# Performance work log

Hardware: AMD Instinct MI355X
Metric: run time of the kernel (lower is better)

## Reference

```python
import jax, jax.numpy as jnp
import numpy as np

N, E, DIN, DOUT, NNZ = 8192, 4096, 256, 128, 65536
TEMP = float(DOUT) ** 0.5
NEG = -1e9


def setup_inputs() -> dict:
    key = jax.random.key(0)
    ks = jax.random.split(key, 8)
    stdv = 1.0 / np.sqrt(DOUT)
    u = lambda k, shp: jax.random.uniform(k, shp, jnp.float32, -stdv, stdv)
    x = jax.random.normal(ks[0], (N, DIN), jnp.float32)
    nodes = jax.random.randint(ks[1], (NNZ,), 0, N, jnp.int32)
    edges = jax.random.randint(ks[2], (NNZ,), 0, E, jnp.int32)
    hyperedge_index = jnp.stack([nodes, edges])  # [2, nnz]
    return {
        "x": x,
        "weight": u(ks[3], (DIN, DOUT)),   # transfer weight
        "weight2": u(ks[4], (DIN, DOUT)),
        "weight3": u(ks[5], (DOUT, DOUT)),
        "bias": u(ks[6], (DOUT,)),
        "q_ctx": u(ks[7], (DOUT,)),        # word_context.weight[0]
        "hyperedge_index": hyperedge_index,
        "num_nodes": N,
        "num_edges": E,
    }


def reference(x, weight, weight2, weight3, bias, q_ctx, hyperedge_index, num_nodes, num_edges):
    # dense incidence H[node, edge] = 1  (hyperedge_preprocess)
    H = jnp.zeros((num_nodes, num_edges), x.dtype).at[
        hyperedge_index[0], hyperedge_index[1]].set(1.0)
    adj = H.T                       # [E, N]  (mask / original attention for attn1)

    x4 = x @ weight2                # [N, D]  x_4att
    xt = x @ weight + bias          # [N, D]  transferred features (v of attn1)

    # ---- attention1: query = shared word-context vector, keys = x4 ----
    row = (q_ctx / TEMP) @ x4.T                    # [N] (q1 rows are identical)
    scores1 = jnp.where(adj == 0, NEG, row[None, :])  # [E, N]
    att1 = jax.nn.softmax(adj, axis=-1) + jax.nn.softmax(scores1, axis=-1)
    edge = att1 @ xt                               # [E, D]

    att2he = att1.T                                # [N, E]

    # ---- attention2: queries = x4, keys = edge @ W3 ----
    edge4 = edge @ weight3                         # [E, D]
    scores2 = jnp.where(adj.T == 0, NEG, (x4 / TEMP) @ edge4.T)  # [N, E]
    att2hn = jax.nn.softmax(adj.T, axis=-1) + jax.nn.softmax(scores2, axis=-1)

    # ---- fused outer-product attention and output projection ----
    A = att2he @ att2he.T + att2hn @ att2hn.T      # [N, N]
    h_prime_g = jax.nn.elu(A @ x4)                 # [N, D]
    return h_prime_g
```

## Files before the change

kernel.cpp:

```cpp
#include <hip/hip_runtime.h>
#include <math.h>

constexpr int Nn   = 8192;
constexpr int Ee   = 4096;
constexpr int DIN  = 256;
constexpr int DOUT = 128;
constexpr int NNZ  = 65536;
constexpr int EC   = 96;
constexpr int NC   = 48;

#define TEMPR 0.08838834764831845f
#define EM1   1.7182818284590452f

typedef __attribute__((ext_vector_type(8))) short short8;
typedef __attribute__((ext_vector_type(4))) float f32x4;

static __device__ __forceinline__ float wave_sum64(float v) {
#pragma unroll
    for (int m = 32; m; m >>= 1) v += __shfl_xor(v, m, 64);
    return v;
}
static __device__ __forceinline__ float wave_max64(float v) {
#pragma unroll
    for (int m = 32; m; m >>= 1) v = fmaxf(v, __shfl_xor(v, m, 64));
    return v;
}
static __device__ __forceinline__ short f2bf(float f) {
    union { float f; unsigned u; } v; v.f = f;
    const unsigned r = (v.u + 0x7FFFu + ((v.u >> 16) & 1u)) >> 16;
    return (short)r;
}
static __device__ __forceinline__ unsigned packbf2(float a, float b) {
    return ((unsigned)(unsigned short)f2bf(a)) |
           (((unsigned)(unsigned short)f2bf(b)) << 16);
}
static __device__ __forceinline__ float2 unpackbf2(unsigned u) {
    union { unsigned u; float f; } lo, hi;
    lo.u = u << 16; hi.u = u & 0xFFFF0000u;
    return make_float2(lo.f, hi.f);
}

__global__ __launch_bounds__(256) void k_ww3(
    const float* __restrict__ W, const float* __restrict__ W2,
    const float* __restrict__ W3, const float* __restrict__ bias,
    short* __restrict__ W2T, short* __restrict__ WWT, float* __restrict__ bW3,
    uint4* __restrict__ zb, unsigned zTot16)
{
    const int b = blockIdx.x;
    const int t = threadIdx.x;
    if (b < 32) {
        __shared__ float sW[8][128];
        const int r0 = b * 8;
        for (int i = t; i < 1024; i += 256)
            sW[i >> 7][i & 127] = W[(size_t)(r0 + (i >> 7)) * DOUT + (i & 127)];
        __syncthreads();
        const int c  = t & 127;
        const int rh = (t >> 7) * 4;
        float acc[4] = {0.f, 0.f, 0.f, 0.f};
        for (int k = 0; k < 128; ++k) {
            const float w3 = W3[(size_t)k * DOUT + c];
#pragma unroll
            for (int i = 0; i < 4; ++i) acc[i] = fmaf(sW[rh + i][k], w3, acc[i]);
        }
#pragma unroll
        for (int i = 0; i < 4; ++i)
            WWT[(size_t)c * DIN + (r0 + rh + i)] = f2bf(acc[i]);
    } else if (b < 40) {
        const int k0 = (b - 32) * 32;
        for (int i = t; i < 32 * 128; i += 256) {
            const int k = k0 + (i >> 7);
            const int n = i & 127;
            W2T[(size_t)n * DIN + k] = f2bf(W2[(size_t)k * DOUT + n]);
        }
    } else if (b == 40) {
        if (t < 128) {
            float acc = 0.f;
            for (int k = 0; k < 128; ++k)
                acc = fmaf(bias[k], W3[(size_t)k * DOUT + t], acc);
            bW3[t] = acc;
        }
    } else {
        uint4 z; z.x = z.y = z.z = z.w = 0u;
        for (unsigned i = (unsigned)(b - 41) * 256u + t; i < zTot16;
             i += 64u * 256u)
            zb[i] = z;
    }
}

__global__ __launch_bounds__(256) void k_gemm1f(
    const float* __restrict__ x, const short* __restrict__ W2T,
    const short* __restrict__ WWT, const float* __restrict__ bW3,
    const float* __restrict__ q, const int* __restrict__ hidx,
    unsigned* __restrict__ bitmap, int* __restrict__ degE, int* __restrict__ degN,
    int* __restrict__ csrEn, int* __restrict__ csrNe, int* __restrict__ csrNs,
    short* __restrict__ x4b, short* __restrict__ xwb,
    float* __restrict__ rowv)
{
    __shared__ float srow[16];
    const int t    = threadIdx.x;
    const int lane = t & 63;
    const int wv   = t >> 6;
    const int n16  = lane & 15;
    const int quad = lane >> 4;
    const int r0   = blockIdx.x * 16;
    const int n0   = wv * 32;

    const unsigned gid = blockIdx.x * 256 + t;
    if (gid < NNZ) {
        const int n = hidx[gid];
        const int e = hidx[NNZ + gid];
        const unsigned word = (unsigned)n * (unsigned)Ee + (unsigned)e;
        const unsigned bit  = 1u << (word & 31u);
        const unsigned old  = atomicOr(&bitmap[word >> 5], bit);
        if (!(old & bit)) {
            const int pe = atomicAdd(&degE[e], 1);
            if (pe < EC) {
                csrEn[e * EC + pe] = n;
                const int pn = atomicAdd(&degN[n], 1);
                if (pn < NC) {
                    csrNe[n * NC + pn] = e;
                    csrNs[n * NC + pn] = e * EC + pe;
                }
            }
        }
    }

    f32x4 acc4[2], accw[2];
#pragma unroll
    for (int nt = 0; nt < 2; ++nt) {
        acc4[nt] = (f32x4){0.f, 0.f, 0.f, 0.f};
        accw[nt] = (f32x4){0.f, 0.f, 0.f, 0.f};
    }
#pragma unroll
    for (int k0 = 0; k0 < DIN; k0 += 32) {
        const int kb = k0 + quad * 8;
        const float4 xa = *(const float4*)&x[(size_t)(r0 + n16) * DIN + kb];
        const float4 xb = *(const float4*)&x[(size_t)(r0 + n16) * DIN + kb + 4];
        short8 af;
        af[0] = f2bf(xa.x); af[1] = f2bf(xa.y); af[2] = f2bf(xa.z); af[3] = f2bf(xa.w);
        af[4] = f2bf(xb.x); af[5] = f2bf(xb.y); af[6] = f2bf(xb.z); af[7] = f2bf(xb.w);
#pragma unroll
        for (int nt = 0; nt < 2; ++nt) {
            const int col = n0 + nt * 16 + n16;
            const short8 b4 = *(const short8*)&W2T[(size_t)col * DIN + kb];
            const short8 bw = *(const short8*)&WWT[(size_t)col * DIN + kb];
            acc4[nt] = __builtin_amdgcn_mfma_f32_16x16x32_bf16(af, b4, acc4[nt], 0, 0, 0);
            accw[nt] = __builtin_amdgcn_mfma_f32_16x16x32_bf16(af, bw, accw[nt], 0, 0, 0);
        }
    }

    float bwv[2], qv[2];
#pragma unroll
    for (int nt = 0; nt < 2; ++nt) {
        const int col = n0 + nt * 16 + n16;
        bwv[nt] = bW3[col];
        qv[nt]  = q[col];
    }
#pragma unroll
    for (int nt = 0; nt < 2; ++nt) {
        const int col = n0 + nt * 16 + n16;
#pragma unroll
        for (int reg = 0; reg < 4; ++reg) {
            const int row = r0 + quad * 4 + reg;
            x4b[(size_t)row * DOUT + col] = f2bf(acc4[nt][reg]);
            xwb[(size_t)row * DOUT + col] = f2bf(accw[nt][reg] + bwv[nt]);
        }
    }
    float pr[4];
#pragma unroll
    for (int reg = 0; reg < 4; ++reg)
        pr[reg] = qv[0] * acc4[0][reg] + qv[1] * acc4[1][reg];
#pragma unroll
    for (int m = 8; m; m >>= 1) {
#pragma unroll
        for (int reg = 0; reg < 4; ++reg) pr[reg] += __shfl_xor(pr[reg], m, 64);
    }
    if (t < 16) srow[t] = 0.f;
    __syncthreads();
    if (n16 == 0) {
#pragma unroll
        for (int reg = 0; reg < 4; ++reg) atomicAdd(&srow[quad * 4 + reg], pr[reg]);
    }
    __syncthreads();
    if (t < 16) rowv[r0 + t] = srow[t] * TEMPR;
}

__global__ __launch_bounds__(256) void k_reduxA(
    const unsigned* __restrict__ x4b, const unsigned* __restrict__ xwb,
    const int* __restrict__ degE,
    float* __restrict__ csx4, float* __restrict__ csxw, float* __restrict__ c2g)
{
    const int t    = threadIdx.x;
    const int lane = t & 63;
    const int w    = t >> 6;
    const int b    = blockIdx.x;
    float2 a4 = {0.f, 0.f}, aw = {0.f, 0.f};
    for (int k = 0; k < 32; ++k) {
        const int n = b * 128 + w + k * 4;
        const float2 fv = unpackbf2(x4b[(size_t)n * 64 + lane]);
        const float2 tv = unpackbf2(xwb[(size_t)n * 64 + lane]);
        a4.x += fv.x; a4.y += fv.y;
        aw.x += tv.x; aw.y += tv.y;
    }
    atomicAdd(&csx4[lane * 2 + 0], a4.x); atomicAdd(&csx4[lane * 2 + 1], a4.y);
    atomicAdd(&csxw[lane * 2 + 0], aw.x); atomicAdd(&csxw[lane * 2 + 1], aw.y);

    const int gid = b * 256 + t;
    if (gid < Ee) {
        const int de = min(degE[gid], EC);
        const float ue = de ? 1.0f / ((float)Nn + (float)de * EM1)
                            : 2.0f / (float)Nn;
        const float v = wave_sum64(ue * ue);
        if (lane == 0) atomicAdd(c2g, v);
    }
}

__global__ __launch_bounds__(256) void k_edge1(
    const int* __restrict__ degE, const int* __restrict__ csrEn,
    const float* __restrict__ rowv,
    const float* __restrict__ csx4, const float* __restrict__ csxw,
    const unsigned* __restrict__ x4b, const unsigned* __restrict__ xwb,
    float* __restrict__ Sval, unsigned* __restrict__ e4b, unsigned* __restrict__ G1b,
    float* __restrict__ wsArr)
{
    __shared__ int   sN[4][EC];
    __shared__ float sS[4][EC];
    const int t    = threadIdx.x;
    const int w    = t >> 6;
    const int lane = t & 63;
    const int e    = blockIdx.x * 4 + w;
    const int deg  = min(degE[e], EC);
    const float ue = deg ? 1.0f / ((float)Nn + (float)deg * EM1) : 2.0f / (float)Nn;

    int   n0 = 0, n1 = 0;
    float r0 = -INFINITY, r1 = -INFINITY;
    if (lane < deg)      { n0 = csrEn[e * EC + lane];      r0 = rowv[n0]; }
    if (lane + 64 < deg) { n1 = csrEn[e * EC + lane + 64]; r1 = rowv[n1]; }
    const float m  = wave_max64(fmaxf(r0, r1));
    const float e0 = (lane < deg)      ? expf(r0 - m) : 0.f;
    const float e1 = (lane + 64 < deg) ? expf(r1 - m) : 0.f;
    const float Z  = wave_sum64(e0 + e1);
    const float inv = deg ? 1.0f / Z : 0.f;
    const float base = EM1 * ue;
    if (lane < deg) {
        const float sv = fmaf(e0, inv, base);
        sN[w][lane] = n0; sS[w][lane] = sv;
        Sval[e * EC + lane] = sv;
        atomicAdd(&wsArr[n0], ue * sv);
    }
    if (lane + 64 < deg) {
        const float sv = fmaf(e1, inv, base);
        sN[w][lane + 64] = n1; sS[w][lane + 64] = sv;
        Sval[e * EC + lane + 64] = sv;
        atomicAdd(&wsArr[n1], ue * sv);
    }

    const float2 cw = *(const float2*)&csxw[lane * 2];
    const float2 c4 = *(const float2*)&csx4[lane * 2];
    float2 aE = make_float2(ue * cw.x, ue * cw.y);
    float2 aG = make_float2(ue * c4.x, ue * c4.y);
    int j = 0;
    for (; j + 8 <= deg; j += 8) {
        int ai[8]; float bi[8]; unsigned tu[8], fu[8];
#pragma unroll
        for (int k = 0; k < 8; ++k) { ai[k] = sN[w][j+k]; bi[k] = sS[w][j+k]; }
#pragma unroll
        for (int k = 0; k < 8; ++k) {
            tu[k] = xwb[(size_t)ai[k] * 64 + lane];
            fu[k] = x4b[(size_t)ai[k] * 64 + lane];
        }
#pragma unroll
        for (int k = 0; k < 8; ++k) {
            const float2 tv = unpackbf2(tu[k]);
            const float2 fv = unpackbf2(fu[k]);
            aE.x = fmaf(bi[k], tv.x, aE.x); aE.y = fmaf(bi[k], tv.y, aE.y);
            aG.x = fmaf(bi[k], fv.x, aG.x); aG.y = fmaf(bi[k], fv.y, aG.y);
        }
    }
    for (; j < deg; ++j) {
        const int   a = sN[w][j];
        const float b = sS[w][j];
        const float2 tv = unpackbf2(xwb[(size_t)a * 64 + lane]);
        const float2 fv = unpackbf2(x4b[(size_t)a * 64 + lane]);
        aE.x = fmaf(b, tv.x, aE.x); aE.y = fmaf(b, tv.y, aE.y);
        aG.x = fmaf(b, fv.x, aG.x); aG.y = fmaf(b, fv.y, aG.y);
    }
    e4b[(size_t)e * 64 + lane] = packbf2(aE.x, aE.y);
    G1b[(size_t)e * 64 + lane] = packbf2(aG.x, aG.y);
}

__global__ __launch_bounds__(256) void k_reduxB(
    const unsigned* __restrict__ x4b, const int* __restrict__ degN,
    const float* __restrict__ wsArr,
    float* __restrict__ vxg, float* __restrict__ twxg, float* __restrict__ wsxg)
{
    const int t    = threadIdx.x;
    const int lane = t & 63;
    const int w    = t >> 6;
    const int b    = blockIdx.x;
    float2 av = {0.f, 0.f}, at2 = {0.f, 0.f}, aw = {0.f, 0.f};
    for (int k = 0; k < 32; ++k) {
        const int n   = b * 128 + w + k * 4;
        const int deg = min(degN[n], NC);
        const float vn = deg ? 1.0f / ((float)Ee + (float)deg * EM1) : 2.0f / (float)Ee;
        const float tw = deg ? fmaf((float)deg * EM1, vn, 1.0f) : 0.f;
        const float wsn = wsArr[n];
        const float2 xv = unpackbf2(x4b[(size_t)n * 64 + lane]);
        av.x  = fmaf(vn,  xv.x, av.x);  av.y  = fmaf(vn,  xv.y, av.y);
        at2.x = fmaf(tw,  xv.x, at2.x); at2.y = fmaf(tw,  xv.y, at2.y);
        aw.x  = fmaf(wsn, xv.x, aw.x);  aw.y  = fmaf(wsn, xv.y, aw.y);
    }
    atomicAdd(&vxg[lane * 2 + 0],  av.x);  atomicAdd(&vxg[lane * 2 + 1],  av.y);
    atomicAdd(&twxg[lane * 2 + 0], at2.x); atomicAdd(&twxg[lane * 2 + 1], at2.y);
    atomicAdd(&wsxg[lane * 2 + 0], aw.x);  atomicAdd(&wsxg[lane * 2 + 1], aw.y);
}

__global__ __launch_bounds__(256) void k_node2(
    const int* __restrict__ degN, const int* __restrict__ csrNe,
    const int* __restrict__ csrNs, const unsigned* __restrict__ x4b,
    const unsigned* __restrict__ e4b,
    float* __restrict__ Tval)
{
    const int t    = threadIdx.x;
    const int w    = t >> 6;
    const int lane = t & 63;
    const int es   = lane >> 3;
    const int dl   = lane & 7;
    const int n    = blockIdx.x * 4 + w;
    const int deg  = min(degN[n], NC);
    if (!deg) return;
    const float vn = 1.0f / ((float)Ee + (float)deg * EM1);

    const uint4* xr = (const uint4*)&x4b[(size_t)n * 64];
    const uint4 xua = xr[dl * 2], xub = xr[dl * 2 + 1];
    const float2 x0 = unpackbf2(xua.x), x1 = unpackbf2(xua.y),
                 x2 = unpackbf2(xua.z), x3 = unpackbf2(xua.w),
                 x4v = unpackbf2(xub.x), x5 = unpackbf2(xub.y),
                 x6 = unpackbf2(xub.z), x7 = unpackbf2(xub.w);

    float dps[6]; float exs[6]; int slots[6];
    float m = -INFINITY;
#pragma unroll
    for (int p = 0; p < 6; ++p) {
        dps[p] = -INFINITY; slots[p] = 0;
        if (p * 8 >= deg) continue;
        const int j = p * 8 + es;
        int ej = 0;
        if (j < deg) { ej = csrNe[n * NC + j]; slots[p] = csrNs[n * NC + j]; }
        const uint4* er = (const uint4*)&e4b[(size_t)ej * 64];
        const uint4 ea = er[dl * 2], eb = er[dl * 2 + 1];
        float d0 = 0.f, d1 = 0.f, d2 = 0.f, d3 = 0.f;
        { const float2 ev = unpackbf2(ea.x); d0 = fmaf(ev.x, x0.x, d0); d0 = fmaf(ev.y, x0.y, d0); }
        { const float2 ev = unpackbf2(ea.y); d1 = fmaf(ev.x, x1.x, d1); d1 = fmaf(ev.y, x1.y, d1); }
        { const float2 ev = unpackbf2(ea.z); d2 = fmaf(ev.x, x2.x, d2); d2 = fmaf(ev.y, x2.y, d2); }
        { const float2 ev = unpackbf2(ea.w); d3 = fmaf(ev.x, x3.x, d3); d3 = fmaf(ev.y, x3.y, d3); }
        { const float2 ev = unpackbf2(eb.x); d0 = fmaf(ev.x, x4v.x, d0); d0 = fmaf(ev.y, x4v.y, d0); }
        { const float2 ev = unpackbf2(eb.y); d1 = fmaf(ev.x, x5.x, d1); d1 = fmaf(ev.y, x5.y, d1); }
        { const float2 ev = unpackbf2(eb.z); d2 = fmaf(ev.x, x6.x, d2); d2 = fmaf(ev.y, x6.y, d2); }
        { const float2 ev = unpackbf2(eb.w); d3 = fmaf(ev.x, x7.x, d3); d3 = fmaf(ev.y, x7.y, d3); }
        float dot = (d0 + d1) + (d2 + d3);
        dot += __shfl_xor(dot, 1, 64);
        dot += __shfl_xor(dot, 2, 64);
        dot += __shfl_xor(dot, 4, 64);
        dot = (j < deg) ? dot * TEMPR : -INFINITY;
        dps[p] = dot;
        float mm = fmaxf(dot, __shfl_xor(dot, 8, 64));
        mm = fmaxf(mm, __shfl_xor(mm, 16, 64));
        mm = fmaxf(mm, __shfl_xor(mm, 32, 64));
        m = fmaxf(m, mm);
    }
    float Z = 0.f;
#pragma unroll
    for (int p = 0; p < 6; ++p) {
        exs[p] = 0.f;
        if (p * 8 >= deg) continue;
        const float ex = (p * 8 + es < deg) ? expf(dps[p] - m) : 0.f;
        exs[p] = ex;
        float s = ex + __shfl_xor(ex, 8, 64);
        s += __shfl_xor(s, 16, 64);
        s += __shfl_xor(s, 32, 64);
        Z += s;
    }
    const float invZ = 1.0f / Z;
#pragma unroll
    for (int p = 0; p < 6; ++p) {
        if (p * 8 >= deg) continue;
        if (dl == 0 && p * 8 + es < deg)
            Tval[slots[p]] = fmaf(EM1, vn, exs[p] * invZ);
    }
}

__global__ __launch_bounds__(256) void k_g2(
    const int* __restrict__ degE, const int* __restrict__ csrEn,
    const float* __restrict__ Tval, const float* __restrict__ vxg,
    const unsigned* __restrict__ x4b, unsigned* __restrict__ G2b)
{
    const int t    = threadIdx.x;
    const int w    = t >> 6;
    const int lane = t & 63;
    const int e    = blockIdx.x * 4 + w;
    const int deg  = min(degE[e], EC);
    float2 acc = *(const float2*)&vxg[lane * 2];
    int j = 0;
    for (; j + 8 <= deg; j += 8) {
        int ai[8]; float bi[8]; unsigned fu[8];
#pragma unroll
        for (int k = 0; k < 8; ++k) { ai[k] = csrEn[e*EC+j+k]; bi[k] = Tval[e*EC+j+k]; }
#pragma unroll
        for (int k = 0; k < 8; ++k)
            fu[k] = x4b[(size_t)ai[k] * 64 + lane];
#pragma unroll
        for (int k = 0; k < 8; ++k) {
            const float2 fv = unpackbf2(fu[k]);
            acc.x = fmaf(bi[k], fv.x, acc.x); acc.y = fmaf(bi[k], fv.y, acc.y);
        }
    }
    for (; j < deg; ++j) {
        const int   a = csrEn[e*EC+j];
        const float b = Tval[e*EC+j];
        const float2 fv = unpackbf2(x4b[(size_t)a * 64 + lane]);
        acc.x = fmaf(b, fv.x, acc.x); acc.y = fmaf(b, fv.y, acc.y);
    }
    G2b[(size_t)e * 64 + lane] = packbf2(acc.x, acc.y);
}

__global__ __launch_bounds__(256) void k_final(
    const int* __restrict__ degN, const int* __restrict__ csrNe,
    const int* __restrict__ csrNs, const float* __restrict__ Sval,
    const float* __restrict__ Tval,
    const float* __restrict__ c2g, const float* __restrict__ csx4,
    const float* __restrict__ wsxg, const float* __restrict__ vxg,
    const float* __restrict__ twxg,
    const unsigned* __restrict__ G1b, const unsigned* __restrict__ G2b,
    float* __restrict__ out)
{
    const int t    = threadIdx.x;
    const int w    = t >> 6;
    const int lane = t & 63;
    const int n    = blockIdx.x * 4 + w;
    const int deg  = min(degN[n], NC);
    const float vn = deg ? 1.0f / ((float)Ee + (float)deg * EM1) : 2.0f / (float)Ee;
    const float c2 = *c2g;
    const float2 c4v = *(const float2*)&csx4[lane * 2];
    const float2 wsv = *(const float2*)&wsxg[lane * 2];
    const float2 vxv = *(const float2*)&vxg[lane * 2];
    const float2 twv = *(const float2*)&twxg[lane * 2];
    float2 acc;
    acc.x = fmaf(c2, c4v.x, wsv.x) + vn * fmaf((float)Ee, vxv.x, twv.x);
    acc.y = fmaf(c2, c4v.y, wsv.y) + vn * fmaf((float)Ee, vxv.y, twv.y);
    int j = 0;
    for (; j + 4 <= deg; j += 4) {
        int ei[4], si[4]; float sv[4], tv[4]; unsigned g1u[4], g2u[4];
#pragma unroll
        for (int k = 0; k < 4; ++k) {
            ei[k] = csrNe[n*NC+j+k]; si[k] = csrNs[n*NC+j+k];
        }
#pragma unroll
        for (int k = 0; k < 4; ++k) {
            sv[k] = Sval[si[k]]; tv[k] = Tval[si[k]];
            g1u[k] = G1b[(size_t)ei[k] * 64 + lane];
            g2u[k] = G2b[(size_t)ei[k] * 64 + lane];
        }
#pragma unroll
        for (int k = 0; k < 4; ++k) {
            const float2 g1 = unpackbf2(g1u[k]);
            const float2 g2 = unpackbf2(g2u[k]);
            acc.x = fmaf(sv[k], g1.x, acc.x); acc.y = fmaf(sv[k], g1.y, acc.y);
            acc.x = fmaf(tv[k], g2.x, acc.x); acc.y = fmaf(tv[k], g2.y, acc.y);
        }
    }
    for (; j < deg; ++j) {
        const int ea = csrNe[n*NC+j];
        const int sa = csrNs[n*NC+j];
        const float sva = Sval[sa], tva = Tval[sa];
        const float2 g1a = unpackbf2(G1b[(size_t)ea * 64 + lane]);
        const float2 g2a = unpackbf2(G2b[(size_t)ea * 64 + lane]);
        acc.x = fmaf(sva, g1a.x, acc.x); acc.y = fmaf(sva, g1a.y, acc.y);
        acc.x = fmaf(tva, g2a.x, acc.x); acc.y = fmaf(tva, g2a.y, acc.y);
    }
    acc.x = acc.x > 0.f ? acc.x : expm1f(acc.x);
    acc.y = acc.y > 0.f ? acc.y : expm1f(acc.y);
    *(float2*)&out[(size_t)n * DOUT + lane * 2] = acc;
}

extern "C" void kernel_launch(void* const* d_in, const int* in_sizes, int n_in,
                              void* d_out, int out_size, void* d_ws, size_t ws_size,
                              hipStream_t stream)
{
    const float* x    = (const float*)d_in[0];
    const float* W    = (const float*)d_in[1];
    const float* W2   = (const float*)d_in[2];
    const float* W3   = (const float*)d_in[3];
    const float* bias = (const float*)d_in[4];
    const float* q    = (const float*)d_in[5];
    const int*   hidx = (const int*)d_in[6];
    float* out = (float*)d_out;

    char* wsp = (char*)d_ws;
    size_t o = 0;
    auto take = [&](size_t bytes) {
        size_t r = o; o += (bytes + 255) & ~(size_t)255; return r;
    };
    unsigned* bitmap = (unsigned*)(wsp + take((size_t)Nn * Ee / 8));
    int*   degE  = (int*)  (wsp + take((size_t)Ee * 4));
    int*   degN  = (int*)  (wsp + take((size_t)Nn * 4));
    float* wsArr = (float*)(wsp + take((size_t)Nn * 4));
    float* c2g   = (float*)(wsp + take(4));
    float* csx4  = (float*)(wsp + take(DOUT * 4));
    float* csxw  = (float*)(wsp + take(DOUT * 4));
    float* vxg   = (float*)(wsp + take(DOUT * 4));
    float* twxg  = (float*)(wsp + take(DOUT * 4));
    float* wsxg  = (float*)(wsp + take(DOUT * 4));
    const size_t zbytes = o;
    short* x4b   = (short*)(wsp + take((size_t)Nn * DOUT * 2));
    short* xwb   = (short*)(wsp + take((size_t)Nn * DOUT * 2));
    float* rowv  = (float*)(wsp + take((size_t)Nn * 4));
    int*   csrEn = (int*)  (wsp + take((size_t)Ee * EC * 4));
    float* Sval  = (float*)(wsp + take((size_t)Ee * EC * 4));
    float* Tval  = (float*)(wsp + take((size_t)Ee * EC * 4));
    int*   csrNe = (int*)  (wsp + take((size_t)Nn * NC * 4));
    int*   csrNs = (int*)  (wsp + take((size_t)Nn * NC * 4));
    unsigned* e4b = (unsigned*)(wsp + take((size_t)Ee * DOUT * 2));
    unsigned* G1b = (unsigned*)(wsp + take((size_t)Ee * DOUT * 2));
    unsigned* G2b = (unsigned*)(wsp + take((size_t)Ee * DOUT * 2));
    short* W2T   = (short*)(wsp + take((size_t)DOUT * DIN * 2));
    short* WWT   = (short*)(wsp + take((size_t)DOUT * DIN * 2));
    float* bW3   = (float*)(wsp + take(DOUT * 4));
    (void)ws_size; (void)in_sizes; (void)n_in; (void)out_size;

    k_ww3   <<<105,     256, 0, stream>>>(W, W2, W3, bias, W2T, WWT, bW3,
                                          (uint4*)d_ws, (unsigned)(zbytes / 16));
    k_gemm1f<<<Nn / 16, 256, 0, stream>>>(x, W2T, WWT, bW3, q, hidx,
                                          bitmap, degE, degN, csrEn, csrNe, csrNs,
                                          x4b, xwb, rowv);
    k_reduxA<<<64,      256, 0, stream>>>((const unsigned*)x4b, (const unsigned*)xwb,
                                          degE, csx4, csxw, c2g);
    k_edge1 <<<Ee / 4,  256, 0, stream>>>(degE, csrEn, rowv, csx4, csxw,
                                          (const unsigned*)x4b, (const unsigned*)xwb,
                                          Sval, e4b, G1b, wsArr);
    k_reduxB<<<64,      256, 0, stream>>>((const unsigned*)x4b, degN, wsArr,
                                          vxg, twxg, wsxg);
    k_node2 <<<Nn / 4,  256, 0, stream>>>(degN, csrNe, csrNs,
                                          (const unsigned*)x4b, e4b, Tval);
    k_g2    <<<Ee / 4,  256, 0, stream>>>(degE, csrEn, Tval, vxg,
                                          (const unsigned*)x4b, G2b);
    k_final <<<Nn / 4,  256, 0, stream>>>(degN, csrNe, csrNs, Sval, Tval,
                                          c2g, csx4, wsxg, vxg, twxg, G1b, G2b, out);
}
```

Baseline: 167.1 us.

## Fuse reduxB into node2, pack bf16 pairs, shrink blocks for gather kernels

Merges the k_reduxB reduction into the k_node2 launch as extra leading blocks, which removes one kernel launch and its dependency gap. Stores x4/xw as packed bf16 pairs of columns (col, col+16) in the GEMM epilogue, so the final output store is remapped to undo the permutation. Shrinks k_edge1, k_g2 and k_final to 128-thread blocks with occupancy hints so more small blocks can be spread across CUs. The permuted layout makes the final writes strided scalar stores instead of float2 stores, and the other kernels must still read these buffers correctly in the new column order.

```diff
diff --git a/kernel.cpp b/kernel.cpp
--- a/kernel.cpp
+++ b/kernel.cpp
@@ -11,6 +11,7 @@
 
 #define TEMPR 0.08838834764831845f
 #define EM1   1.7182818284590452f
+
 
 typedef __attribute__((ext_vector_type(8))) short short8;
 typedef __attribute__((ext_vector_type(4))) float f32x4;
@@ -93,7 +94,7 @@
     const float* __restrict__ q, const int* __restrict__ hidx,
     unsigned* __restrict__ bitmap, int* __restrict__ degE, int* __restrict__ degN,
     int* __restrict__ csrEn, int* __restrict__ csrNe, int* __restrict__ csrNs,
-    short* __restrict__ x4b, short* __restrict__ xwb,
+    unsigned* __restrict__ x4b, unsigned* __restrict__ xwb,
     float* __restrict__ rowv)
 {
     __shared__ float srow[16];
@@ -156,15 +157,13 @@
         bwv[nt] = bW3[col];
         qv[nt]  = q[col];
     }
-#pragma unroll
-    for (int nt = 0; nt < 2; ++nt) {
-        const int col = n0 + nt * 16 + n16;
-#pragma unroll
-        for (int reg = 0; reg < 4; ++reg) {
-            const int row = r0 + quad * 4 + reg;
-            x4b[(size_t)row * DOUT + col] = f2bf(acc4[nt][reg]);
-            xwb[(size_t)row * DOUT + col] = f2bf(accw[nt][reg] + bwv[nt]);
-        }
+    const int s = wv * 16 + n16;
+#pragma unroll
+    for (int reg = 0; reg < 4; ++reg) {
+        const int row = r0 + quad * 4 + reg;
+        x4b[(size_t)row * 64 + s] = packbf2(acc4[0][reg], acc4[1][reg]);
+        xwb[(size_t)row * 64 + s] = packbf2(accw[0][reg] + bwv[0],
+                                            accw[1][reg] + bwv[1]);
     }
     float pr[4];
 #pragma unroll
@@ -215,7 +214,7 @@
     }
 }
 
-__global__ __launch_bounds__(256) void k_edge1(
+__global__ __launch_bounds__(128, 6) void k_edge1(
     const int* __restrict__ degE, const int* __restrict__ csrEn,
     const float* __restrict__ rowv,
     const float* __restrict__ csx4, const float* __restrict__ csxw,
@@ -223,12 +222,12 @@
     float* __restrict__ Sval, unsigned* __restrict__ e4b, unsigned* __restrict__ G1b,
     float* __restrict__ wsArr)
 {
-    __shared__ int   sN[4][EC];
-    __shared__ float sS[4][EC];
+    __shared__ int   sN[2][EC];
+    __shared__ float sS[2][EC];
     const int t    = threadIdx.x;
     const int w    = t >> 6;
     const int lane = t & 63;
-    const int e    = blockIdx.x * 4 + w;
+    const int e    = blockIdx.x * 2 + w;
     const int deg  = min(degE[e], EC);
     const float ue = deg ? 1.0f / ((float)Nn + (float)deg * EM1) : 2.0f / (float)Nn;
 
@@ -289,44 +288,41 @@
     G1b[(size_t)e * 64 + lane] = packbf2(aG.x, aG.y);
 }
 
-__global__ __launch_bounds__(256) void k_reduxB(
-    const unsigned* __restrict__ x4b, const int* __restrict__ degN,
-    const float* __restrict__ wsArr,
-    float* __restrict__ vxg, float* __restrict__ twxg, float* __restrict__ wsxg)
-{
-    const int t    = threadIdx.x;
-    const int lane = t & 63;
-    const int w    = t >> 6;
-    const int b    = blockIdx.x;
-    float2 av = {0.f, 0.f}, at2 = {0.f, 0.f}, aw = {0.f, 0.f};
-    for (int k = 0; k < 32; ++k) {
-        const int n   = b * 128 + w + k * 4;
-        const int deg = min(degN[n], NC);
-        const float vn = deg ? 1.0f / ((float)Ee + (float)deg * EM1) : 2.0f / (float)Ee;
-        const float tw = deg ? fmaf((float)deg * EM1, vn, 1.0f) : 0.f;
-        const float wsn = wsArr[n];
-        const float2 xv = unpackbf2(x4b[(size_t)n * 64 + lane]);
-        av.x  = fmaf(vn,  xv.x, av.x);  av.y  = fmaf(vn,  xv.y, av.y);
-        at2.x = fmaf(tw,  xv.x, at2.x); at2.y = fmaf(tw,  xv.y, at2.y);
-        aw.x  = fmaf(wsn, xv.x, aw.x);  aw.y  = fmaf(wsn, xv.y, aw.y);
-    }
-    atomicAdd(&vxg[lane * 2 + 0],  av.x);  atomicAdd(&vxg[lane * 2 + 1],  av.y);
-    atomicAdd(&twxg[lane * 2 + 0], at2.x); atomicAdd(&twxg[lane * 2 + 1], at2.y);
-    atomicAdd(&wsxg[lane * 2 + 0], aw.x);  atomicAdd(&wsxg[lane * 2 + 1], aw.y);
-}
-
-__global__ __launch_bounds__(256) void k_node2(
+__global__ __launch_bounds__(256) void k_nodeB(
     const int* __restrict__ degN, const int* __restrict__ csrNe,
     const int* __restrict__ csrNs, const unsigned* __restrict__ x4b,
-    const unsigned* __restrict__ e4b,
-    float* __restrict__ Tval)
+    const unsigned* __restrict__ e4b, const float* __restrict__ wsArr,
+    float* __restrict__ Tval,
+    float* __restrict__ vxg, float* __restrict__ twg, float* __restrict__ wsg)
 {
     const int t    = threadIdx.x;
     const int w    = t >> 6;
     const int lane = t & 63;
+    const int b    = blockIdx.x;
+
+    if (b < 64) {
+        float2 av = {0.f, 0.f}, at2 = {0.f, 0.f}, aw = {0.f, 0.f};
+        for (int k = 0; k < 32; ++k) {
+            const int n   = b * 128 + w + k * 4;
+            const int deg = min(degN[n], NC);
+            const float vn = deg ? 1.0f / ((float)Ee + (float)deg * EM1)
+                                 : 2.0f / (float)Ee;
+            const float tw = deg ? fmaf((float)deg * EM1, vn, 1.0f) : 0.f;
+            const float wsn = wsArr[n];
+            const float2 xv = unpackbf2(x4b[(size_t)n * 64 + lane]);
+            av.x  = fmaf(vn,  xv.x, av.x);  av.y  = fmaf(vn,  xv.y, av.y);
+            at2.x = fmaf(tw,  xv.x, at2.x); at2.y = fmaf(tw,  xv.y, at2.y);
+            aw.x  = fmaf(wsn, xv.x, aw.x);  aw.y  = fmaf(wsn, xv.y, aw.y);
+        }
+        atomicAdd(&vxg[lane*2+0], av.x);  atomicAdd(&vxg[lane*2+1], av.y);
+        atomicAdd(&twg[lane*2+0], at2.x); atomicAdd(&twg[lane*2+1], at2.y);
+        atomicAdd(&wsg[lane*2+0], aw.x);  atomicAdd(&wsg[lane*2+1], aw.y);
+        return;
+    }
+
     const int es   = lane >> 3;
     const int dl   = lane & 7;
-    const int n    = blockIdx.x * 4 + w;
+    const int n    = (b - 64) * 4 + w;
     const int deg  = min(degN[n], NC);
     if (!deg) return;
     const float vn = 1.0f / ((float)Ee + (float)deg * EM1);
@@ -376,10 +372,10 @@
         if (p * 8 >= deg) continue;
         const float ex = (p * 8 + es < deg) ? expf(dps[p] - m) : 0.f;
         exs[p] = ex;
-        float s = ex + __shfl_xor(ex, 8, 64);
-        s += __shfl_xor(s, 16, 64);
-        s += __shfl_xor(s, 32, 64);
-        Z += s;
+        float sum = ex + __shfl_xor(ex, 8, 64);
+        sum += __shfl_xor(sum, 16, 64);
+        sum += __shfl_xor(sum, 32, 64);
+        Z += sum;
     }
     const float invZ = 1.0f / Z;
 #pragma unroll
@@ -390,7 +386,7 @@
     }
 }
 
-__global__ __launch_bounds__(256) void k_g2(
+__global__ __launch_bounds__(128, 8) void k_g2(
     const int* __restrict__ degE, const int* __restrict__ csrEn,
     const float* __restrict__ Tval, const float* __restrict__ vxg,
     const unsigned* __restrict__ x4b, unsigned* __restrict__ G2b)
@@ -398,7 +394,7 @@
     const int t    = threadIdx.x;
     const int w    = t >> 6;
     const int lane = t & 63;
-    const int e    = blockIdx.x * 4 + w;
+    const int e    = blockIdx.x * 2 + w;
     const int deg  = min(degE[e], EC);
     float2 acc = *(const float2*)&vxg[lane * 2];
     int j = 0;
@@ -424,27 +420,27 @@
     G2b[(size_t)e * 64 + lane] = packbf2(acc.x, acc.y);
 }
 
-__global__ __launch_bounds__(256) void k_final(
+__global__ __launch_bounds__(128, 6) void k_final(
     const int* __restrict__ degN, const int* __restrict__ csrNe,
     const int* __restrict__ csrNs, const float* __restrict__ Sval,
     const float* __restrict__ Tval,
     const float* __restrict__ c2g, const float* __restrict__ csx4,
-    const float* __restrict__ wsxg, const float* __restrict__ vxg,
-    const float* __restrict__ twxg,
+    const float* __restrict__ wsg, const float* __restrict__ vxg,
+    const float* __restrict__ twg,
     const unsigned* __restrict__ G1b, const unsigned* __restrict__ G2b,
     float* __restrict__ out)
 {
     const int t    = threadIdx.x;
     const int w    = t >> 6;
     const int lane = t & 63;
-    const int n    = blockIdx.x * 4 + w;
+    const int n    = blockIdx.x * 2 + w;
     const int deg  = min(degN[n], NC);
     const float vn = deg ? 1.0f / ((float)Ee + (float)deg * EM1) : 2.0f / (float)Ee;
     const float c2 = *c2g;
     const float2 c4v = *(const float2*)&csx4[lane * 2];
-    const float2 wsv = *(const float2*)&wsxg[lane * 2];
+    const float2 wsv = *(const float2*)&wsg[lane * 2];
     const float2 vxv = *(const float2*)&vxg[lane * 2];
-    const float2 twv = *(const float2*)&twxg[lane * 2];
+    const float2 twv = *(const float2*)&twg[lane * 2];
     float2 acc;
     acc.x = fmaf(c2, c4v.x, wsv.x) + vn * fmaf((float)Ee, vxv.x, twv.x);
     acc.y = fmaf(c2, c4v.y, wsv.y) + vn * fmaf((float)Ee, vxv.y, twv.y);
@@ -480,7 +476,9 @@
     }
     acc.x = acc.x > 0.f ? acc.x : expm1f(acc.x);
     acc.y = acc.y > 0.f ? acc.y : expm1f(acc.y);
-    *(float2*)&out[(size_t)n * DOUT + lane * 2] = acc;
+    const int lo = ((lane >> 4) << 5) + (lane & 15);
+    out[(size_t)n * DOUT + lo]      = acc.x;
+    out[(size_t)n * DOUT + lo + 16] = acc.y;
 }
 
 extern "C" void kernel_launch(void* const* d_in, const int* in_sizes, int n_in,
@@ -509,41 +507,36 @@
     float* csx4  = (float*)(wsp + take(DOUT * 4));
     float* csxw  = (float*)(wsp + take(DOUT * 4));
     float* vxg   = (float*)(wsp + take(DOUT * 4));
-    float* twxg  = (float*)(wsp + take(DOUT * 4));
-    float* wsxg  = (float*)(wsp + take(DOUT * 4));
+    float* twg   = (float*)(wsp + take(DOUT * 4));
+    float* wsg   = (float*)(wsp + take(DOUT * 4));
     const size_t zbytes = o;
-    short* x4b   = (short*)(wsp + take((size_t)Nn * DOUT * 2));
-    short* xwb   = (short*)(wsp + take((size_t)Nn * DOUT * 2));
-    float* rowv  = (float*)(wsp + take((size_t)Nn * 4));
-    int*   csrEn = (int*)  (wsp + take((size_t)Ee * EC * 4));
-    float* Sval  = (float*)(wsp + take((size_t)Ee * EC * 4));
-    float* Tval  = (float*)(wsp + take((size_t)Ee * EC * 4));
-    int*   csrNe = (int*)  (wsp + take((size_t)Nn * NC * 4));
-    int*   csrNs = (int*)  (wsp + take((size_t)Nn * NC * 4));
-    unsigned* e4b = (unsigned*)(wsp + take((size_t)Ee * DOUT * 2));
-    unsigned* G1b = (unsigned*)(wsp + take((size_t)Ee * DOUT * 2));
-    unsigned* G2b = (unsigned*)(wsp + take((size_t)Ee * DOUT * 2));
-    short* W2T   = (short*)(wsp + take((size_t)DOUT * DIN * 2));
-    short* WWT   = (short*)(wsp + take((size_t)DOUT * DIN * 2));
-    float* bW3   = (float*)(wsp + take(DOUT * 4));
+    unsigned* x4b   = (unsigned*)(wsp + take((size_t)Nn * 64 * 4));
+    unsigned* xwb   = (unsigned*)(wsp + take((size_t)Nn * 64 * 4));
+    float*    rowv  = (float*)   (wsp + take((size_t)Nn * 4));
+    int*      csrEn = (int*)     (wsp + take((size_t)Ee * EC * 4));
+    float*    Sval  = (float*)   (wsp + take((size_t)Ee * EC * 4));
+    float*    Tval  = (float*)   (wsp + take((size_t)Ee * EC * 4));
+    int*      csrNe = (int*)     (wsp + take((size_t)Nn * NC * 4));
+    int*      csrNs = (int*)     (wsp + take((size_t)Nn * NC * 4));
+    unsigned* e4b   = (unsigned*)(wsp + take((size_t)Ee * 64 * 4));
+    unsigned* G1b   = (unsigned*)(wsp + take((size_t)Ee * 64 * 4));
+    unsigned* G2b   = (unsigned*)(wsp + take((size_t)Ee * 64 * 4));
+    short*    W2T   = (short*)   (wsp + take((size_t)DOUT * DIN * 2));
+    short*    WWT   = (short*)   (wsp + take((size_t)DOUT * DIN * 2));
+    float*    bW3   = (float*)   (wsp + take(DOUT * 4));
     (void)ws_size; (void)in_sizes; (void)n_in; (void)out_size;
 
-    k_ww3   <<<105,     256, 0, stream>>>(W, W2, W3, bias, W2T, WWT, bW3,
-                                          (uint4*)d_ws, (unsigned)(zbytes / 16));
-    k_gemm1f<<<Nn / 16, 256, 0, stream>>>(x, W2T, WWT, bW3, q, hidx,
-                                          bitmap, degE, degN, csrEn, csrNe, csrNs,
-                                          x4b, xwb, rowv);
-    k_reduxA<<<64,      256, 0, stream>>>((const unsigned*)x4b, (const unsigned*)xwb,
-                                          degE, csx4, csxw, c2g);
-    k_edge1 <<<Ee / 4,  256, 0, stream>>>(degE, csrEn, rowv, csx4, csxw,
-                                          (const unsigned*)x4b, (const unsigned*)xwb,
-                                          Sval, e4b, G1b, wsArr);
-    k_reduxB<<<64,      256, 0, stream>>>((const unsigned*)x4b, degN, wsArr,
-                                          vxg, twxg, wsxg);
-    k_node2 <<<Nn / 4,  256, 0, stream>>>(degN, csrNe, csrNs,
-                                          (const unsigned*)x4b, e4b, Tval);
-    k_g2    <<<Ee / 4,  256, 0, stream>>>(degE, csrEn, Tval, vxg,
-                                          (const unsigned*)x4b, G2b);
-    k_final <<<Nn / 4,  256, 0, stream>>>(degN, csrNe, csrNs, Sval, Tval,
-                                          c2g, csx4, wsxg, vxg, twxg, G1b, G2b, out);
-}
+    k_ww3   <<<105,       256, 0, stream>>>(W, W2, W3, bias, W2T, WWT, bW3,
+                                            (uint4*)d_ws, (unsigned)(zbytes / 16));
+    k_gemm1f<<<Nn / 16,   256, 0, stream>>>(x, W2T, WWT, bW3, q, hidx,
+                                            bitmap, degE, degN, csrEn, csrNe, csrNs,
+                                            x4b, xwb, rowv);
+    k_reduxA<<<64,        256, 0, stream>>>(x4b, xwb, degE, csx4, csxw, c2g);
+    k_edge1 <<<Ee / 2,    128, 0, stream>>>(degE, csrEn, rowv, csx4, csxw,
+                                            x4b, xwb, Sval, e4b, G1b, wsArr);
+    k_nodeB <<<64 + Nn/4, 256, 0, stream>>>(degN, csrNe, csrNs, x4b, e4b, wsArr,
+                                            Tval, vxg, twg, wsg);
+    k_g2    <<<Ee / 2,    128, 0, stream>>>(degE, csrEn, Tval, vxg, x4b, G2b);
+    k_final <<<Nn / 2,    128, 0, stream>>>(degN, csrNe, csrNs, Sval, Tval,
+                                            c2g, csx4, wsg, vxg, twg, G1b, G2b, out);
+}
```

Result: no change. 164.2 us (-1.7%).
